# Kernel tuning notes

Hardware: AMD Instinct MI355X
Metric: run time of the kernel (lower is better)

## Reference

```python
import jax, jax.numpy as jnp
import numpy as np

D_STATE = 4096
D_CONV = 16
T_IN = D_STATE - D_CONV + 1  # forced: conv output length (T + d_conv - 1) must equal d_state


def setup_inputs() -> dict:
    key = jax.random.key(0)
    ks = jax.random.split(key, 6)
    x = jax.random.normal(ks[0], (1, T_IN, 1), dtype=jnp.float32)
    conv_w = jax.random.normal(ks[1], (D_STATE, 1, D_CONV), dtype=jnp.float32) * 0.25
    conv_b = jax.random.normal(ks[2], (D_STATE,), dtype=jnp.float32) * 0.1
    # A param shifted negative so a = sum(exp(A*time_decay)) < 1; the original
    # randn init makes the d_state-step geometric recurrence overflow to inf
    # for large d_state, which would make correctness comparison meaningless.
    A_p = jax.random.normal(ks[3], (D_STATE,), dtype=jnp.float32) * 0.1 - 10.0
    time_decay = jnp.full((D_STATE,), 0.95, dtype=jnp.float32)
    proj_w = jax.random.normal(ks[4], (D_STATE,), dtype=jnp.float32) * 0.02  # Conv1d(C,1,1) weight, squeezed
    proj_b = jax.random.normal(ks[5], (1,), dtype=jnp.float32) * 0.01
    return dict(x=x, conv_w=conv_w, conv_b=conv_b, A_p=A_p,
                time_decay=time_decay, proj_w=proj_w, proj_b=proj_b)


def reference(x, conv_w, conv_b, A_p, time_decay, proj_w, proj_b):
    # x: (B=1, T, 1)
    S = A_p.shape[0]
    pad = D_CONV - 1
    # Conv1d(1, S, kernel=D_CONV, padding=D_CONV-1): output length T + D_CONV - 1 == S
    xc = jax.lax.conv_general_dilated(
        x.transpose(0, 2, 1), conv_w, window_strides=(1,),
        padding=[(pad, pad)], dimension_numbers=('NCH', 'OIH', 'NCH'))
    xc = (xc + conv_b[None, :, None]).transpose(0, 2, 1)  # (B, S, C) with C == S

    A = jnp.exp(A_p * time_decay)  # (S,)
    # torch loop: s_0 = xc; s_k = (A @ s_{k-1}) + xc  (A@s contracts the length dim,
    # result (B, C) broadcasts back over length). With u_k := A @ s_k and a := sum(A):
    #   u_0 = A @ xc,  u_k = a * u_{k-1} + u_0,  s_k = u_{k-1}[:, None, :] + xc
    # so sum(s_0..s_S) = (S+1)*xc + sum_{k=0}^{S-1} u_k  -- exact, no (B,S,C) carries.
    u0 = jnp.einsum('s,bsc->bc', A, xc)  # (B, C)
    a = A.sum()

    def step(carry, _):
        u, acc = carry
        return (a * u + u0, acc + u), None

    (_, acc), _ = jax.lax.scan(step, (u0, jnp.zeros_like(u0)), None, length=S)
    x_combined = (S + 1) * xc + acc[:, None, :]  # (B, S, C)

    # output_proj: Conv1d(C, 1, kernel=1) applied along the length dim
    out = jnp.einsum('bsc,c->bs', x_combined, proj_w) + proj_b  # (B, S)
    return out[:, None, :]  # (B, 1, S)
```

## Files before the change

kernel.cpp:

```cpp
#include <hip/hip_runtime.h>
#include <math.h>

#define SDIM 4096
#define TLEN 4081
#define DC   16

#define NB1  64
#define NT1  64
#define NB2  16
#define NT2  256
#define NVAL 34



__global__ __launch_bounds__(NT1) void k1_partials(
    const float* __restrict__ x, const float* __restrict__ conv_w,
    const float* __restrict__ conv_b, const float* __restrict__ A_p,
    const float* __restrict__ td, const float* __restrict__ pw,
    float* __restrict__ ws)
{
    __shared__ float xt[NT1 + DC];
    const int t = threadIdx.x;
    const int b = blockIdx.x;
    const int s = b * NT1 + t;

    for (int i = t; i < NT1 + DC; i += NT1) {
        int j = b * NT1 + i - (DC - 1);
        xt[i] = (j >= 0 && j < TLEN) ? x[j] : 0.0f;
    }

    const float p = pw[s];
    const float4* wrow = (const float4*)(conv_w + (size_t)s * DC);
    float4 w0 = wrow[0], w1 = wrow[1], w2 = wrow[2], w3 = wrow[3];
    float wk[DC] = { w0.x*p, w0.y*p, w0.z*p, w0.w*p,
                     w1.x*p, w1.y*p, w1.z*p, w1.w*p,
                     w2.x*p, w2.y*p, w2.z*p, w2.w*p,
                     w3.x*p, w3.y*p, w3.z*p, w3.w*p };
    float bs = conv_b[s] * p;
    float ea = expf(A_p[s] * td[s]);

    __syncthreads();
    float h[DC];
#pragma unroll
    for (int k = 0; k < DC; ++k) h[k] = ea * xt[t + k];

#pragma unroll
    for (int off = 32; off >= 1; off >>= 1) {
#pragma unroll
        for (int k = 0; k < DC; ++k) { wk[k] += __shfl_xor(wk[k], off);
                                       h[k]  += __shfl_xor(h[k],  off); }
        bs += __shfl_xor(bs, off);
        ea += __shfl_xor(ea, off);
    }
    if (t == 0) {
#pragma unroll
        for (int k = 0; k < DC; ++k) { ws[k * NB1 + b]        = wk[k];
                                       ws[(DC + k) * NB1 + b] = h[k]; }
        ws[32 * NB1 + b] = bs;
        ws[33 * NB1 + b] = ea;
    }
}

__global__ __launch_bounds__(NT2) void k2_final(
    const float* __restrict__ x, const float* __restrict__ pb,
    const float* __restrict__ ws, float* __restrict__ out)
{
    __shared__ float red[NVAL];
    __shared__ float xt[NT2 + DC];
    __shared__ float Ksh;
    const int t = threadIdx.x;
    const int b = blockIdx.x;

    if (t < NVAL) {
        const float* col = ws + t * NB1;
        float v = 0.0f;
#pragma unroll
        for (int i = 0; i < NB1; ++i) v += col[i];
        red[t] = v;
    }
    for (int i = t; i < NT2 + DC - 1; i += NT2) {
        int j = b * NT2 + i - (DC - 1);
        xt[i] = (j >= 0 && j < TLEN) ? x[j] : 0.0f;
    }
    __syncthreads();

    if (t == 0) {
        float day = red[32] * red[33];
#pragma unroll
        for (int k = 0; k < DC; ++k) day += red[k] * red[DC + k];
        double ad  = (double)red[33];
        double omA = 1.0 - ad;
        double aS  = (ad > 0.9999) ? exp((double)SDIM * log(ad)) : 0.0;
        double G   = ((double)SDIM - ad * (1.0 - aS) / omA) / omA;
        Ksh = (float)(G * (double)day + (double)pb[0]);
    }
    __syncthreads();

    float wkr[DC];
#pragma unroll
    for (int k = 0; k < DC; ++k) wkr[k] = red[k];
    const float bsum = red[32];
    const float K    = Ksh;

    float acc = bsum;
#pragma unroll
    for (int k = 0; k < DC; ++k) acc += xt[t + k] * wkr[k];
    out[b * NT2 + t] = (float)(SDIM + 1) * acc + K;
}

extern "C" void kernel_launch(void* const* d_in, const int* in_sizes, int n_in,
                              void* d_out, int out_size, void* d_ws, size_t ws_size,
                              hipStream_t stream) {
    const float* x      = (const float*)d_in[0];
    const float* conv_w = (const float*)d_in[1];
    const float* conv_b = (const float*)d_in[2];
    const float* A_p    = (const float*)d_in[3];
    const float* td     = (const float*)d_in[4];
    const float* pw     = (const float*)d_in[5];
    const float* pb     = (const float*)d_in[6];
    float* ws = (float*)d_ws;

    k1_partials<<<NB1, NT1, 0, stream>>>(x, conv_w, conv_b, A_p, td, pw, ws);
    k2_final<<<NB2, NT2, 0, stream>>>(x, pb, ws, (float*)d_out);
}
```

Before: 12.10 us.

## Fuse two kernels into one cooperative kernel with grid-wide sync

```diff
diff --git a/kernel.cpp b/kernel.cpp
--- a/kernel.cpp
+++ b/kernel.cpp
@@ -1,31 +1,34 @@
 #include <hip/hip_runtime.h>
+#include <hip/hip_cooperative_groups.h>
 #include <math.h>
+
+namespace cg = cooperative_groups;
 
 #define SDIM 4096
 #define TLEN 4081
 #define DC   16
 
-#define NB1  64
-#define NT1  64
-#define NB2  16
-#define NT2  256
+#define NB   64
+#define NT   64
 #define NVAL 34
 
 
-
-__global__ __launch_bounds__(NT1) void k1_partials(
+__global__ __launch_bounds__(NT) void mamba_coop(
     const float* __restrict__ x, const float* __restrict__ conv_w,
     const float* __restrict__ conv_b, const float* __restrict__ A_p,
     const float* __restrict__ td, const float* __restrict__ pw,
-    float* __restrict__ ws)
+    const float* __restrict__ pb, float* __restrict__ ws,
+    float* __restrict__ out)
 {
-    __shared__ float xt[NT1 + DC];
+    __shared__ float xt[NT + DC];
+    __shared__ float red[NVAL];
+    __shared__ float Ksh;
     const int t = threadIdx.x;
     const int b = blockIdx.x;
-    const int s = b * NT1 + t;
+    const int s = b * NT + t;
 
-    for (int i = t; i < NT1 + DC; i += NT1) {
-        int j = b * NT1 + i - (DC - 1);
+    for (int i = t; i < NT + DC; i += NT) {
+        int j = b * NT + i - (DC - 1);
         xt[i] = (j >= 0 && j < TLEN) ? x[j] : 0.0f;
     }
 
@@ -54,33 +57,20 @@
     }
     if (t == 0) {
 #pragma unroll
-        for (int k = 0; k < DC; ++k) { ws[k * NB1 + b]        = wk[k];
-                                       ws[(DC + k) * NB1 + b] = h[k]; }
-        ws[32 * NB1 + b] = bs;
-        ws[33 * NB1 + b] = ea;
+        for (int k = 0; k < DC; ++k) { ws[k * NB + b]        = wk[k];
+                                       ws[(DC + k) * NB + b] = h[k]; }
+        ws[32 * NB + b] = bs;
+        ws[33 * NB + b] = ea;
     }
-}
 
-__global__ __launch_bounds__(NT2) void k2_final(
-    const float* __restrict__ x, const float* __restrict__ pb,
-    const float* __restrict__ ws, float* __restrict__ out)
-{
-    __shared__ float red[NVAL];
-    __shared__ float xt[NT2 + DC];
-    __shared__ float Ksh;
-    const int t = threadIdx.x;
-    const int b = blockIdx.x;
+    cg::this_grid().sync();
 
     if (t < NVAL) {
-        const float* col = ws + t * NB1;
+        const float* col = ws + t * NB;
         float v = 0.0f;
 #pragma unroll
-        for (int i = 0; i < NB1; ++i) v += col[i];
+        for (int i = 0; i < NB; ++i) v += col[i];
         red[t] = v;
-    }
-    for (int i = t; i < NT2 + DC - 1; i += NT2) {
-        int j = b * NT2 + i - (DC - 1);
-        xt[i] = (j >= 0 && j < TLEN) ? x[j] : 0.0f;
     }
     __syncthreads();
 
@@ -105,7 +95,7 @@
     float acc = bsum;
 #pragma unroll
     for (int k = 0; k < DC; ++k) acc += xt[t + k] * wkr[k];
-    out[b * NT2 + t] = (float)(SDIM + 1) * acc + K;
+    out[s] = (float)(SDIM + 1) * acc + K;
 }
 
 extern "C" void kernel_launch(void* const* d_in, const int* in_sizes, int n_in,
@@ -118,8 +108,10 @@
     const float* td     = (const float*)d_in[4];
     const float* pw     = (const float*)d_in[5];
     const float* pb     = (const float*)d_in[6];
-    float* ws = (float*)d_ws;
+    float* ws  = (float*)d_ws;
+    float* out = (float*)d_out;
 
-    k1_partials<<<NB1, NT1, 0, stream>>>(x, conv_w, conv_b, A_p, td, pw, ws);
-    k2_final<<<NB2, NT2, 0, stream>>>(x, pb, ws, (float*)d_out);
+    void* args[] = { &x, &conv_w, &conv_b, &A_p, &td, &pw, &pb, &ws, &out };
+    hipLaunchCooperativeKernel((const void*)mamba_coop, dim3(NB), dim3(NT),
+                               args, 0, stream);
 }
```

After: 38.40 us. 3.17x slower.
